# Kernel tuning notes

Hardware: AMD Instinct MI355X
Metric: run time of the kernel (lower is better)

## Reference

```python
import jax, jax.numpy as jnp
import numpy as np

N_NODES = 100000
N_EDGES = 800000
N_LAYERS = 6
GATE_TYPES = 29
H = 256        # hidden dim
INTER = 256    # inter dim
EDGE_F = 3     # (src_idx, dst_idx, reversed) edge features


def setup_inputs() -> dict:
    key = jax.random.key(0)
    ks = jax.random.split(key, 16)
    gate_type = jax.random.randint(ks[0], (N_NODES,), 0, GATE_TYPES)
    src = jax.random.randint(ks[1], (N_EDGES,), 0, N_NODES)
    dst = jax.random.randint(ks[2], (N_EDGES,), 0, N_NODES)
    w = jax.random.uniform(ks[3], (N_EDGES, EDGE_F), dtype=jnp.float32)
    s = 0.05
    emb = jax.random.normal(ks[4], (GATE_TYPES, H), dtype=jnp.float32) * s
    # QConv per layer: linear1 (no bias): [INTER, H+3]; linear2: [H, H+INTER] + bias
    W1 = jax.random.normal(ks[5], (N_LAYERS, INTER, H + EDGE_F), dtype=jnp.float32) * s
    W2 = jax.random.normal(ks[6], (N_LAYERS, H, H + INTER), dtype=jnp.float32) * s
    b2 = jax.random.normal(ks[7], (N_LAYERS, H), dtype=jnp.float32) * s
    # MLP head 256->256->1
    Wh1 = jax.random.normal(ks[8], (H, H), dtype=jnp.float32) * s
    bh1 = jax.random.normal(ks[9], (H,), dtype=jnp.float32) * s
    Wh2 = jax.random.normal(ks[10], (1, H), dtype=jnp.float32) * s
    bh2 = jax.random.normal(ks[11], (1,), dtype=jnp.float32) * s
    return {"gate_type": gate_type, "src": src, "dst": dst, "w": w,
            "emb": emb, "W1": W1, "W2": W2, "b2": b2,
            "Wh1": Wh1, "bh1": bh1, "Wh2": Wh2, "bh2": bh2}


def reference(gate_type, src, dst, w, emb, W1, W2, b2, Wh1, bh1, Wh2, bh2):
    n = gate_type.shape[0]
    h = emb[gate_type]                                   # [N, H]
    deg = jax.ops.segment_sum(jnp.ones((src.shape[0],), h.dtype), dst, num_segments=n)
    inv_deg = (1.0 / jnp.maximum(deg, 1.0))[:, None]      # mean over mailbox; 0-deg nodes -> h_N = 0
    for l in range(W1.shape[0]):
        m = jnp.concatenate([h[src], w], axis=1)          # [E, H+3] gather
        tmp = jax.nn.leaky_relu(m @ W1[l].T, 0.01)        # [E, INTER]
        h_N = jax.ops.segment_sum(tmp, dst, num_segments=n) * inv_deg  # scatter-mean [N, INTER]
        h = jax.nn.relu(jnp.concatenate([h, h_N], axis=1) @ W2[l].T + b2[l])
    x = jax.nn.relu(h @ Wh1.T + bh1)                      # [N, H]
    return x @ Wh2.T + bh2                                # [N, 1]
```

## Files before the change

### kernel.cpp

```cpp
#include <hip/hip_runtime.h>

#define H 256
#define NLAYERS 6
typedef unsigned int uint32;
typedef unsigned short u16;

typedef __bf16 bf16;
typedef bf16 bf16x8 __attribute__((ext_vector_type(8)));
typedef float f32x4 __attribute__((ext_vector_type(4)));
typedef u16 u16x8 __attribute__((ext_vector_type(8)));

__device__ __forceinline__ float bf2f(u16 h) {
    return __uint_as_float(((uint32)h) << 16);
}
__device__ __forceinline__ u16 f2bf(float f) {
    uint32 u = __float_as_uint(f);
    u = u + 0x7FFFu + ((u >> 16) & 1u);
    return (u16)(u >> 16);
}

__device__ __forceinline__ void glds16(const void* src, const char* ldsdst) {
    __builtin_amdgcn_global_load_lds(
        (const __attribute__((address_space(1))) void*)src,
        (__attribute__((address_space(3))) void*)ldsdst, 16, 0, 0);
}


__global__ __launch_bounds__(256)
void count_kernel(const int* __restrict__ dst, int* __restrict__ deg, int E) {
    int e = blockIdx.x * 256 + threadIdx.x;
    if (e < E) atomicAdd(&deg[dst[e]], 1);
}

__global__ __launch_bounds__(256)
void invd_kernel(const int* __restrict__ deg, float* __restrict__ invd, int N) {
    int n = blockIdx.x * 256 + threadIdx.x;
    if (n < N) invd[n] = 1.f / fmaxf((float)deg[n], 1.f);
}

__global__ __launch_bounds__(256)
void scan1_kernel(const int* __restrict__ deg, int* __restrict__ bsum, int N) {
    __shared__ int s[256];
    int t = threadIdx.x;
    int i = blockIdx.x * 256 + t;
    s[t] = (i < N) ? deg[i] : 0;
    __syncthreads();
    for (int off = 128; off; off >>= 1) {
        if (t < off) s[t] += s[t + off];
        __syncthreads();
    }
    if (t == 0) bsum[blockIdx.x] = s[0];
}

__global__ __launch_bounds__(512)
void scan2_kernel(int* __restrict__ bsum, int nb) {
    __shared__ int s[512];
    int t = threadIdx.x;
    int v = (t < nb) ? bsum[t] : 0;
    s[t] = v;
    __syncthreads();
    for (int off = 1; off < 512; off <<= 1) {
        int x = (t >= off) ? s[t - off] : 0;
        __syncthreads();
        s[t] += x;
        __syncthreads();
    }
    if (t < nb) bsum[t] = s[t] - v;
}

__global__ __launch_bounds__(256)
void scan3_kernel(const int* __restrict__ deg, const int* __restrict__ bsum,
                  int* __restrict__ rowptr, int N, int E) {
    __shared__ int s[256];
    int t = threadIdx.x;
    int i = blockIdx.x * 256 + t;
    int v = (i < N) ? deg[i] : 0;
    s[t] = v;
    __syncthreads();
    for (int off = 1; off < 256; off <<= 1) {
        int x = (t >= off) ? s[t - off] : 0;
        __syncthreads();
        s[t] += x;
        __syncthreads();
    }
    if (i < N) rowptr[i] = s[t] - v + bsum[blockIdx.x];
    if (i == 0) rowptr[N] = E;
}

__global__ __launch_bounds__(256)
void scatter_kernel(const int* __restrict__ src, const int* __restrict__ dst,
                    const float* __restrict__ w, const int* __restrict__ rowptr,
                    int* __restrict__ cursor, int* __restrict__ srcS,
                    float* __restrict__ wS, int E) {
    int e = blockIdx.x * 256 + threadIdx.x;
    if (e >= E) return;
    int d = dst[e];
    int p = rowptr[d] + atomicAdd(&cursor[d], 1);
    srcS[p] = src[e];
    float4 wq;
    wq.x = w[(size_t)e * 3 + 0];
    wq.y = w[(size_t)e * 3 + 1];
    wq.z = w[(size_t)e * 3 + 2];
    wq.w = 0.f;
    *(float4*)&wS[(size_t)p * 4] = wq;
}


__global__ __launch_bounds__(256)
void wsplit_kernel(const float* __restrict__ W1, const float* __restrict__ W2,
                   const float* __restrict__ Wh1,
                   u16* __restrict__ W1hi, u16* __restrict__ W1lo,
                   u16* __restrict__ W2hi, u16* __restrict__ W2lo,
                   u16* __restrict__ Wh1hi, u16* __restrict__ Wh1lo)
{
    int i = blockIdx.x * 256 + threadIdx.x;
    float v; u16* ph; u16* pl; int o;
    if (i < 393216) {
        int l = i >> 16, rem = i & 65535, r = rem >> 8, k = rem & 255;
        v = W1[(size_t)l * 66304 + (size_t)r * 259 + k];
        ph = W1hi; pl = W1lo; o = i;
    } else if (i < 1179648) {
        int j = i - 393216;
        v = W2[j];
        ph = W2hi; pl = W2lo; o = j;
    } else if (i < 1245184) {
        int j = i - 1179648;
        v = Wh1[j];
        ph = Wh1hi; pl = Wh1lo; o = j;
    } else return;
    u16 hi = f2bf(v);
    ph[o] = hi;
    pl[o] = f2bf(v - bf2f(hi));
}

__global__ void extract_kernel(const float* __restrict__ W1, float* __restrict__ ccAll)
{
    int l = blockIdx.x;
    int i = threadIdx.x;
    const float* W1l = W1 + (size_t)l * 66304;
    float* cc = ccAll + (size_t)l * 768;
    #pragma unroll
    for (int j = 0; j < 3; ++j)
        cc[j * 256 + i] = W1l[(size_t)i * 259 + 256 + j];
}


__global__ __launch_bounds__(256)
void emb_split_kernel(const int* __restrict__ gt, const float* __restrict__ emb,
                      u16* __restrict__ hHi, u16* __restrict__ hLo, int N) {
    size_t idx = (size_t)blockIdx.x * 256 + threadIdx.x;
    if (idx >= (size_t)N * 256) return;
    int n = (int)(idx >> 8), c = (int)(idx & 255);
    float v = emb[(size_t)gt[n] * 256 + c];
    u16 hi = f2bf(v);
    hHi[idx] = hi;
    hLo[idx] = f2bf(v - bf2f(hi));
}


#define LDS_AHI 0
#define LDS_ALO 8192
#define LDS_WHI 16384
#define LDS_WLO 32768
#define BUFSZ   49152

template<bool MAIN>
__device__ __forceinline__ void do_compute(const char* B, const int* aoff,
                                           const int* woff, f32x4 (&acc)[4][4]) {
    bf16x8 ah[4], al[4];
    #pragma unroll
    for (int mi = 0; mi < 4; ++mi) {
        ah[mi] = *(const bf16x8*)(B + LDS_AHI + aoff[mi]);
        if (MAIN) al[mi] = *(const bf16x8*)(B + LDS_ALO + aoff[mi]);
    }
    #pragma unroll
    for (int nj = 0; nj < 4; ++nj) {
        bf16x8 wh = *(const bf16x8*)(B + LDS_WHI + woff[nj]);
        bf16x8 wl = *(const bf16x8*)(B + LDS_WLO + woff[nj]);
        #pragma unroll
        for (int mi = 0; mi < 4; ++mi) {
            acc[mi][nj] = __builtin_amdgcn_mfma_f32_16x16x32_bf16(wh, ah[mi], acc[mi][nj], 0, 0, 0);
            acc[mi][nj] = __builtin_amdgcn_mfma_f32_16x16x32_bf16(wl, ah[mi], acc[mi][nj], 0, 0, 0);
            if (MAIN)
                acc[mi][nj] = __builtin_amdgcn_mfma_f32_16x16x32_bf16(wh, al[mi], acc[mi][nj], 0, 0, 0);
        }
    }
}

template<int KTOT, bool BIASRELU, bool WLO>
__global__ __launch_bounds__(512)
void mfma_gemm_kernel(const u16* __restrict__ Ahi_, const u16* __restrict__ Alo_,
                      const u16* __restrict__ A2_,
                      const u16* __restrict__ Whi_, const u16* __restrict__ Wlo_,
                      const float* __restrict__ bias,
                      u16* __restrict__ Chi, u16* __restrict__ Clo, int M)
{
    __shared__ __align__(128) char lds[2 * BUFSZ];
    const int tid = threadIdx.x;
    const int wv = tid >> 6;
    const int lane = tid & 63;
    const int m0 = blockIdx.x * 128;
    const int lrow = lane & 15, koct = lane >> 4;
    const int rh = wv & 1, cg = wv >> 1;

    int aoff[4], woff[4];
    #pragma unroll
    for (int mi = 0; mi < 4; ++mi) {
        int r = rh * 64 + mi * 16 + lrow;
        aoff[mi] = r * 64 + ((koct ^ ((r >> 1) & 3)) << 4);
    }
    #pragma unroll
    for (int nj = 0; nj < 4; ++nj) {
        int r = cg * 64 + nj * 16 + lrow;
        woff[nj] = r * 64 + ((koct ^ ((r >> 1) & 3)) << 4);
    }

    const int arow = tid >> 2;
    const int achk = (tid & 3) ^ ((arow >> 1) & 3);
    const long agrow = (long)((m0 + arow < M) ? (m0 + arow) : (M - 1));
    const char* Asrc_hi = (const char*)Ahi_ + agrow * 512 + achk * 16;
    const char* Asrc_lo = (const char*)Alo_ + agrow * 512 + achk * 16;
    const char* Asrc_2  = (const char*)A2_  + agrow * 512 + achk * 16;

    int wrow0 = tid >> 2,          wchk0 = (tid & 3) ^ ((wrow0 >> 1) & 3);
    int wrow1 = (512 + tid) >> 2,  wchk1 = ((512 + tid) & 3) ^ ((wrow1 >> 1) & 3);
    const char* Wsrc_h0 = (const char*)Whi_ + (long)wrow0 * (KTOT * 2) + wchk0 * 16;
    const char* Wsrc_h1 = (const char*)Whi_ + (long)wrow1 * (KTOT * 2) + wchk1 * 16;
    const char* Wsrc_l0 = (const char*)Wlo_ + (long)wrow0 * (KTOT * 2) + wchk0 * 16;
    const char* Wsrc_l1 = (const char*)Wlo_ + (long)wrow1 * (KTOT * 2) + wchk1 * 16;

    auto STAGE = [&](char* B, int t) {
        const int k0 = t * 32;
        if (KTOT == 256 || k0 < 256) {
            glds16(Asrc_hi + k0 * 2, B + LDS_AHI + wv * 1024);
            glds16(Asrc_lo + k0 * 2, B + LDS_ALO + wv * 1024);
        } else {
            glds16(Asrc_2 + (k0 - 256) * 2, B + LDS_AHI + wv * 1024);
        }
        glds16(Wsrc_h0 + k0 * 2, B + LDS_WHI + wv * 1024);
        glds16(Wsrc_h1 + k0 * 2, B + LDS_WHI + 8192 + wv * 1024);
        glds16(Wsrc_l0 + k0 * 2, B + LDS_WLO + wv * 1024);
        glds16(Wsrc_l1 + k0 * 2, B + LDS_WLO + 8192 + wv * 1024);
    };

    f32x4 acc[4][4] = {};

    char* bcur = lds;
    char* bnxt = lds + BUFSZ;

    STAGE(bcur, 0);
    asm volatile("s_waitcnt vmcnt(0)" ::: "memory");
    __builtin_amdgcn_s_barrier();
    __builtin_amdgcn_sched_barrier(0);

    const int NT = KTOT / 32;
    for (int t = 0; t < NT; ++t) {
        if (t + 1 < NT) STAGE(bnxt, t + 1);
        if (KTOT == 256 || t < 8) do_compute<true>(bcur, aoff, woff, acc);
        else                      do_compute<false>(bcur, aoff, woff, acc);
        asm volatile("s_waitcnt lgkmcnt(0) vmcnt(0)" ::: "memory");
        __builtin_amdgcn_s_barrier();
        __builtin_amdgcn_sched_barrier(0);
        char* z = bcur; bcur = bnxt; bnxt = z;
    }

    float4 bv[4];
    if (BIASRELU) {
        #pragma unroll
        for (int nj = 0; nj < 4; ++nj)
            bv[nj] = *(const float4*)&bias[cg * 64 + nj * 16 + koct * 4];
    }
    #pragma unroll
    for (int mi = 0; mi < 4; ++mi) {
        int row = m0 + rh * 64 + mi * 16 + lrow;
        if (row >= M) continue;
        #pragma unroll
        for (int nj = 0; nj < 4; ++nj) {
            f32x4 v = acc[mi][nj];
            if (BIASRELU) {
                v[0] = fmaxf(v[0] + bv[nj].x, 0.f);
                v[1] = fmaxf(v[1] + bv[nj].y, 0.f);
                v[2] = fmaxf(v[2] + bv[nj].z, 0.f);
                v[3] = fmaxf(v[3] + bv[nj].w, 0.f);
            }
            size_t o = (size_t)row * 256 + cg * 64 + nj * 16 + koct * 4;
            ushort4 ohi;
            ohi.x = f2bf(v[0]); ohi.y = f2bf(v[1]);
            ohi.z = f2bf(v[2]); ohi.w = f2bf(v[3]);
            *(ushort4*)&Chi[o] = ohi;
            if (WLO) {
                ushort4 olo;
                olo.x = f2bf(v[0] - bf2f(ohi.x));
                olo.y = f2bf(v[1] - bf2f(ohi.y));
                olo.z = f2bf(v[2] - bf2f(ohi.z));
                olo.w = f2bf(v[3] - bf2f(ohi.w));
                *(ushort4*)&Clo[o] = olo;
            }
        }
    }
}


__global__ __launch_bounds__(256)
void edge_agg_kernel(const int* __restrict__ rowptr, const int* __restrict__ srcS,
                     const float* __restrict__ wS, const u16* __restrict__ T,
                     const float* __restrict__ cc, const float* __restrict__ invd,
                     u16* __restrict__ hN, int N) {
    int n = blockIdx.x * 4 + (threadIdx.x >> 6);
    int lane = threadIdx.x & 63;
    if (n >= N) return;
    const int half = lane >> 5;
    const int c32 = lane & 31;
    const int col0 = c32 * 8;

    float c0[8], c1[8], c2[8];
    #pragma unroll
    for (int j = 0; j < 3; ++j) {
        float4 lo4 = *(const float4*)&cc[j * 256 + col0];
        float4 hi4 = *(const float4*)&cc[j * 256 + col0 + 4];
        float* cj = (j == 0) ? c0 : (j == 1) ? c1 : c2;
        cj[0] = lo4.x; cj[1] = lo4.y; cj[2] = lo4.z; cj[3] = lo4.w;
        cj[4] = hi4.x; cj[5] = hi4.y; cj[6] = hi4.z; cj[7] = hi4.w;
    }

    float acc[8] = {};
    const int e0 = rowptr[n], e1 = rowptr[n + 1];
    int e = e0 + half;
    for (; e + 6 < e1; e += 8) {
        int s0 = srcS[e], s1 = srcS[e + 2], s2 = srcS[e + 4], s3 = srcS[e + 6];
        float4 wa = *(const float4*)&wS[(size_t)e * 4];
        float4 wb = *(const float4*)&wS[(size_t)(e + 2) * 4];
        float4 wc = *(const float4*)&wS[(size_t)(e + 4) * 4];
        float4 wd = *(const float4*)&wS[(size_t)(e + 6) * 4];
        u16x8 t0 = *(const u16x8*)&T[(size_t)s0 * 256 + col0];
        u16x8 t1 = *(const u16x8*)&T[(size_t)s1 * 256 + col0];
        u16x8 t2 = *(const u16x8*)&T[(size_t)s2 * 256 + col0];
        u16x8 t3 = *(const u16x8*)&T[(size_t)s3 * 256 + col0];
        #pragma unroll
        for (int q = 0; q < 8; ++q) {
            float x0 = fmaf(wa.x, c0[q], fmaf(wa.y, c1[q], fmaf(wa.z, c2[q], bf2f(t0[q]))));
            acc[q] += (x0 > 0.f) ? x0 : 0.01f * x0;
            float x1 = fmaf(wb.x, c0[q], fmaf(wb.y, c1[q], fmaf(wb.z, c2[q], bf2f(t1[q]))));
            acc[q] += (x1 > 0.f) ? x1 : 0.01f * x1;
            float x2 = fmaf(wc.x, c0[q], fmaf(wc.y, c1[q], fmaf(wc.z, c2[q], bf2f(t2[q]))));
            acc[q] += (x2 > 0.f) ? x2 : 0.01f * x2;
            float x3 = fmaf(wd.x, c0[q], fmaf(wd.y, c1[q], fmaf(wd.z, c2[q], bf2f(t3[q]))));
            acc[q] += (x3 > 0.f) ? x3 : 0.01f * x3;
        }
    }
    for (; e < e1; e += 2) {
        int s0 = srcS[e];
        float4 wa = *(const float4*)&wS[(size_t)e * 4];
        u16x8 t0 = *(const u16x8*)&T[(size_t)s0 * 256 + col0];
        #pragma unroll
        for (int q = 0; q < 8; ++q) {
            float x = fmaf(wa.x, c0[q], fmaf(wa.y, c1[q], fmaf(wa.z, c2[q], bf2f(t0[q]))));
            acc[q] += (x > 0.f) ? x : 0.01f * x;
        }
    }
    #pragma unroll
    for (int q = 0; q < 8; ++q) acc[q] += __shfl_xor(acc[q], 32);
    if (half == 0) {
        float sc = invd[n];
        u16x8 o;
        #pragma unroll
        for (int q = 0; q < 8; ++q) o[q] = f2bf(acc[q] * sc);
        *(u16x8*)&hN[(size_t)n * 256 + col0] = o;
    }
}


__global__ __launch_bounds__(256)
void head_out_kernel(const u16* __restrict__ xhi, const u16* __restrict__ xlo,
                     const float* __restrict__ wh2,
                     const float* __restrict__ bh2, float* __restrict__ out, int N) {
    int n = blockIdx.x * 4 + (threadIdx.x >> 6);
    int lane = threadIdx.x & 63;
    if (n >= N) return;
    ushort4 hv = ((const ushort4*)(xhi + (size_t)n * H))[lane];
    ushort4 lv = ((const ushort4*)(xlo + (size_t)n * H))[lane];
    float4 wv = ((const float4*)wh2)[lane];
    float x0 = bf2f(hv.x) + bf2f(lv.x);
    float x1 = bf2f(hv.y) + bf2f(lv.y);
    float x2 = bf2f(hv.z) + bf2f(lv.z);
    float x3 = bf2f(hv.w) + bf2f(lv.w);
    float sum = x0 * wv.x + x1 * wv.y + x2 * wv.z + x3 * wv.w;
    #pragma unroll
    for (int off = 32; off; off >>= 1) sum += __shfl_xor(sum, off);
    if (lane == 0) out[n] = sum + bh2[0];
}


extern "C" void kernel_launch(void* const* d_in, const int* in_sizes, int n_in,
                              void* d_out, int out_size, void* d_ws, size_t ws_size,
                              hipStream_t stream) {
    const int*   gate_type = (const int*)d_in[0];
    const int*   src  = (const int*)d_in[1];
    const int*   dst  = (const int*)d_in[2];
    const float* w    = (const float*)d_in[3];
    const float* emb  = (const float*)d_in[4];
    const float* W1   = (const float*)d_in[5];
    const float* W2   = (const float*)d_in[6];
    const float* b2   = (const float*)d_in[7];
    const float* Wh1  = (const float*)d_in[8];
    const float* bh1  = (const float*)d_in[9];
    const float* Wh2  = (const float*)d_in[10];
    const float* bh2  = (const float*)d_in[11];
    float* out = (float*)d_out;

    const int N = in_sizes[0];
    const int E = in_sizes[1];

    char* p = (char*)d_ws;
    auto alloc = [&](size_t bytes) -> char* {
        char* r = p;
        p += (bytes + 1023) & ~(size_t)1023;
        return r;
    };
    u16*   hHi   = (u16*)  alloc((size_t)N * H * 2);
    u16*   hLo   = (u16*)  alloc((size_t)N * H * 2);
    u16*   tBuf  = (u16*)  alloc((size_t)N * H * 2);
    u16*   hNBuf = (u16*)  alloc((size_t)N * H * 2);
    int*   srcS  = (int*)  alloc((size_t)E * 4);
    float* wS    = (float*)alloc((size_t)E * 4 * 4);
    int*   rowptr= (int*)  alloc((size_t)(N + 1) * 4);
    int*   cursor= (int*)  alloc((size_t)N * 4);
    int*   bsum  = (int*)  alloc(4096);
    float* invd  = (float*)alloc((size_t)N * 4);
    float* ccAll = (float*)alloc(6u * 768 * 4);
    u16*   W1hi  = (u16*)  alloc(6u * 256 * 256 * 2);
    u16*   W1lo  = (u16*)  alloc(6u * 256 * 256 * 2);
    u16*   W2hi  = (u16*)  alloc(6u * 256 * 512 * 2);
    u16*   W2lo  = (u16*)  alloc(6u * 256 * 512 * 2);
    u16*   Wh1hi = (u16*)  alloc(256u * 256 * 2);
    u16*   Wh1lo = (u16*)  alloc(256u * 256 * 2);

    const int nb1 = (N + 255) / 256;

    hipMemsetAsync(cursor, 0, (size_t)N * 4, stream);
    count_kernel<<<(E + 255) / 256, 256, 0, stream>>>(dst, cursor, E);
    invd_kernel<<<nb1, 256, 0, stream>>>(cursor, invd, N);
    scan1_kernel<<<nb1, 256, 0, stream>>>(cursor, bsum, N);
    scan2_kernel<<<1, 512, 0, stream>>>(bsum, nb1);
    scan3_kernel<<<nb1, 256, 0, stream>>>(cursor, bsum, rowptr, N, E);
    hipMemsetAsync(cursor, 0, (size_t)N * 4, stream);
    scatter_kernel<<<(E + 255) / 256, 256, 0, stream>>>(src, dst, w, rowptr, cursor, srcS, wS, E);

    wsplit_kernel<<<4864, 256, 0, stream>>>(W1, W2, Wh1, W1hi, W1lo, W2hi, W2lo, Wh1hi, Wh1lo);
    extract_kernel<<<6, 256, 0, stream>>>(W1, ccAll);
    emb_split_kernel<<<N, 256, 0, stream>>>(gate_type, emb, hHi, hLo, N);

    const int gm = (N + 127) / 128;
    for (int l = 0; l < NLAYERS; ++l) {
        mfma_gemm_kernel<256, false, false><<<gm, 512, 0, stream>>>(
            hHi, hLo, nullptr, W1hi + (size_t)l * 65536, W1lo + (size_t)l * 65536,
            nullptr, tBuf, nullptr, N);
        edge_agg_kernel<<<(N + 3) / 4, 256, 0, stream>>>(
            rowptr, srcS, wS, tBuf, ccAll + (size_t)l * 768, invd, hNBuf, N);
        mfma_gemm_kernel<512, true, true><<<gm, 512, 0, stream>>>(
            hHi, hLo, hNBuf, W2hi + (size_t)l * 131072, W2lo + (size_t)l * 131072,
            b2 + (size_t)l * 256, hHi, hLo, N);
    }
    mfma_gemm_kernel<256, true, true><<<gm, 512, 0, stream>>>(
        hHi, hLo, nullptr, Wh1hi, Wh1lo, bh1, hHi, hLo, N);
    head_out_kernel<<<(N + 3) / 4, 256, 0, stream>>>(hHi, hLo, Wh2, bh2, out, N);
}
```

Before: 1.936 ms.

## Load GEMM A operand straight to registers and make GEMM kernel persistent

The MFMA GEMM no longer stages the activation (A) tiles through LDS. Each lane reads its bf16x8 hi/lo fragments directly from global memory, and LDS now double-buffers only the hi/lo weight tiles, which halves the LDS footprint. The kernel becomes persistent: a fixed grid of 512 blocks strides over the 128-row tiles, and launch bounds now request 4 blocks per CU. The aim is to cut LDS traffic and usage and raise occupancy. The risks are that the direct A loads are only partially coalesced and get no prefetch, so their global latency sits exposed behind the per-step vmcnt(0) wait.

```diff
diff --git a/kernel.cpp b/kernel.cpp
--- a/kernel.cpp
+++ b/kernel.cpp
@@ -158,25 +158,16 @@
 }
 
 
-#define LDS_AHI 0
-#define LDS_ALO 8192
-#define LDS_WHI 16384
-#define LDS_WLO 32768
-#define BUFSZ   49152
+#define WBUF 32768
 
 template<bool MAIN>
-__device__ __forceinline__ void do_compute(const char* B, const int* aoff,
-                                           const int* woff, f32x4 (&acc)[4][4]) {
-    bf16x8 ah[4], al[4];
-    #pragma unroll
-    for (int mi = 0; mi < 4; ++mi) {
-        ah[mi] = *(const bf16x8*)(B + LDS_AHI + aoff[mi]);
-        if (MAIN) al[mi] = *(const bf16x8*)(B + LDS_ALO + aoff[mi]);
-    }
+__device__ __forceinline__ void do_compute(const char* B, const int* woff,
+                                           const bf16x8* ah, const bf16x8* al,
+                                           f32x4 (&acc)[4][4]) {
     #pragma unroll
     for (int nj = 0; nj < 4; ++nj) {
-        bf16x8 wh = *(const bf16x8*)(B + LDS_WHI + woff[nj]);
-        bf16x8 wl = *(const bf16x8*)(B + LDS_WLO + woff[nj]);
+        bf16x8 wh = *(const bf16x8*)(B + woff[nj]);
+        bf16x8 wl = *(const bf16x8*)(B + 16384 + woff[nj]);
         #pragma unroll
         for (int mi = 0; mi < 4; ++mi) {
             acc[mi][nj] = __builtin_amdgcn_mfma_f32_16x16x32_bf16(wh, ah[mi], acc[mi][nj], 0, 0, 0);
@@ -188,113 +179,119 @@
 }
 
 template<int KTOT, bool BIASRELU, bool WLO>
-__global__ __launch_bounds__(512)
+__global__ __launch_bounds__(512, 4)
 void mfma_gemm_kernel(const u16* __restrict__ Ahi_, const u16* __restrict__ Alo_,
                       const u16* __restrict__ A2_,
                       const u16* __restrict__ Whi_, const u16* __restrict__ Wlo_,
                       const float* __restrict__ bias,
-                      u16* __restrict__ Chi, u16* __restrict__ Clo, int M)
+                      u16* __restrict__ Chi, u16* __restrict__ Clo,
+                      int M, int ntiles)
 {
-    __shared__ __align__(128) char lds[2 * BUFSZ];
+    __shared__ __align__(128) char lds[2 * WBUF];
     const int tid = threadIdx.x;
     const int wv = tid >> 6;
     const int lane = tid & 63;
-    const int m0 = blockIdx.x * 128;
     const int lrow = lane & 15, koct = lane >> 4;
     const int rh = wv & 1, cg = wv >> 1;
-
-    int aoff[4], woff[4];
-    #pragma unroll
-    for (int mi = 0; mi < 4; ++mi) {
-        int r = rh * 64 + mi * 16 + lrow;
-        aoff[mi] = r * 64 + ((koct ^ ((r >> 1) & 3)) << 4);
-    }
+    const int NT = KTOT / 32;
+
+    int woff[4];
     #pragma unroll
     for (int nj = 0; nj < 4; ++nj) {
         int r = cg * 64 + nj * 16 + lrow;
         woff[nj] = r * 64 + ((koct ^ ((r >> 1) & 3)) << 4);
     }
 
-    const int arow = tid >> 2;
-    const int achk = (tid & 3) ^ ((arow >> 1) & 3);
-    const long agrow = (long)((m0 + arow < M) ? (m0 + arow) : (M - 1));
-    const char* Asrc_hi = (const char*)Ahi_ + agrow * 512 + achk * 16;
-    const char* Asrc_lo = (const char*)Alo_ + agrow * 512 + achk * 16;
-    const char* Asrc_2  = (const char*)A2_  + agrow * 512 + achk * 16;
-
-    int wrow0 = tid >> 2,          wchk0 = (tid & 3) ^ ((wrow0 >> 1) & 3);
-    int wrow1 = (512 + tid) >> 2,  wchk1 = ((512 + tid) & 3) ^ ((wrow1 >> 1) & 3);
-    const char* Wsrc_h0 = (const char*)Whi_ + (long)wrow0 * (KTOT * 2) + wchk0 * 16;
-    const char* Wsrc_h1 = (const char*)Whi_ + (long)wrow1 * (KTOT * 2) + wchk1 * 16;
-    const char* Wsrc_l0 = (const char*)Wlo_ + (long)wrow0 * (KTOT * 2) + wchk0 * 16;
-    const char* Wsrc_l1 = (const char*)Wlo_ + (long)wrow1 * (KTOT * 2) + wchk1 * 16;
-
-    auto STAGE = [&](char* B, int t) {
-        const int k0 = t * 32;
-        if (KTOT == 256 || k0 < 256) {
-            glds16(Asrc_hi + k0 * 2, B + LDS_AHI + wv * 1024);
-            glds16(Asrc_lo + k0 * 2, B + LDS_ALO + wv * 1024);
-        } else {
-            glds16(Asrc_2 + (k0 - 256) * 2, B + LDS_AHI + wv * 1024);
-        }
-        glds16(Wsrc_h0 + k0 * 2, B + LDS_WHI + wv * 1024);
-        glds16(Wsrc_h1 + k0 * 2, B + LDS_WHI + 8192 + wv * 1024);
-        glds16(Wsrc_l0 + k0 * 2, B + LDS_WLO + wv * 1024);
-        glds16(Wsrc_l1 + k0 * 2, B + LDS_WLO + 8192 + wv * 1024);
-    };
-
-    f32x4 acc[4][4] = {};
-
-    char* bcur = lds;
-    char* bnxt = lds + BUFSZ;
-
-    STAGE(bcur, 0);
-    asm volatile("s_waitcnt vmcnt(0)" ::: "memory");
-    __builtin_amdgcn_s_barrier();
-    __builtin_amdgcn_sched_barrier(0);
-
-    const int NT = KTOT / 32;
-    for (int t = 0; t < NT; ++t) {
-        if (t + 1 < NT) STAGE(bnxt, t + 1);
-        if (KTOT == 256 || t < 8) do_compute<true>(bcur, aoff, woff, acc);
-        else                      do_compute<false>(bcur, aoff, woff, acc);
-        asm volatile("s_waitcnt lgkmcnt(0) vmcnt(0)" ::: "memory");
+    const int wrow0 = tid >> 2;
+    const int wchk0 = (tid & 3) ^ ((wrow0 >> 1) & 3);
+    const int wrow1 = 128 + (tid >> 2);
+    const int wchk1 = (tid & 3) ^ ((wrow1 >> 1) & 3);
+    const uint32 wsrc0 = (uint32)wrow0 * (KTOT * 2) + wchk0 * 16;
+    const uint32 wsrc1 = (uint32)wrow1 * (KTOT * 2) + wchk1 * 16;
+    const int ldst = wv * 1024;
+
+    for (int tile = blockIdx.x; tile < ntiles; tile += gridDim.x) {
+        const int m0 = tile * 128;
+
+        uint32 aoffB[4];
+        #pragma unroll
+        for (int mi = 0; mi < 4; ++mi) {
+            int row = m0 + rh * 64 + mi * 16 + lrow;
+            if (row > M - 1) row = M - 1;
+            aoffB[mi] = ((uint32)row * 256 + (uint32)koct * 8) * 2;
+        }
+
+        f32x4 acc[4][4] = {};
+
+        glds16((const char*)Whi_ + wsrc0, lds + ldst);
+        glds16((const char*)Whi_ + wsrc1, lds + 8192 + ldst);
+        glds16((const char*)Wlo_ + wsrc0, lds + 16384 + ldst);
+        glds16((const char*)Wlo_ + wsrc1, lds + 24576 + ldst);
+        asm volatile("s_waitcnt vmcnt(0)" ::: "memory");
         __builtin_amdgcn_s_barrier();
         __builtin_amdgcn_sched_barrier(0);
-        char* z = bcur; bcur = bnxt; bnxt = z;
-    }
-
-    float4 bv[4];
-    if (BIASRELU) {
-        #pragma unroll
-        for (int nj = 0; nj < 4; ++nj)
-            bv[nj] = *(const float4*)&bias[cg * 64 + nj * 16 + koct * 4];
-    }
-    #pragma unroll
-    for (int mi = 0; mi < 4; ++mi) {
-        int row = m0 + rh * 64 + mi * 16 + lrow;
-        if (row >= M) continue;
-        #pragma unroll
-        for (int nj = 0; nj < 4; ++nj) {
-            f32x4 v = acc[mi][nj];
-            if (BIASRELU) {
-                v[0] = fmaxf(v[0] + bv[nj].x, 0.f);
-                v[1] = fmaxf(v[1] + bv[nj].y, 0.f);
-                v[2] = fmaxf(v[2] + bv[nj].z, 0.f);
-                v[3] = fmaxf(v[3] + bv[nj].w, 0.f);
+
+        #pragma unroll
+        for (int t = 0; t < NT; ++t) {
+            const char* bcur = lds + (t & 1) * WBUF;
+            char* bnxt = lds + ((t + 1) & 1) * WBUF;
+            if (t + 1 < NT) {
+                glds16((const char*)Whi_ + wsrc0 + (t + 1) * 64, bnxt + ldst);
+                glds16((const char*)Whi_ + wsrc1 + (t + 1) * 64, bnxt + 8192 + ldst);
+                glds16((const char*)Wlo_ + wsrc0 + (t + 1) * 64, bnxt + 16384 + ldst);
+                glds16((const char*)Wlo_ + wsrc1 + (t + 1) * 64, bnxt + 24576 + ldst);
             }
-            size_t o = (size_t)row * 256 + cg * 64 + nj * 16 + koct * 4;
-            ushort4 ohi;
-            ohi.x = f2bf(v[0]); ohi.y = f2bf(v[1]);
-            ohi.z = f2bf(v[2]); ohi.w = f2bf(v[3]);
-            *(ushort4*)&Chi[o] = ohi;
-            if (WLO) {
-                ushort4 olo;
-                olo.x = f2bf(v[0] - bf2f(ohi.x));
-                olo.y = f2bf(v[1] - bf2f(ohi.y));
-                olo.z = f2bf(v[2] - bf2f(ohi.z));
-                olo.w = f2bf(v[3] - bf2f(ohi.w));
-                *(ushort4*)&Clo[o] = olo;
+            bf16x8 ah[4], al[4];
+            if (KTOT == 256 || t < 8) {
+                #pragma unroll
+                for (int mi = 0; mi < 4; ++mi) {
+                    ah[mi] = *(const bf16x8*)((const char*)Ahi_ + aoffB[mi] + t * 64);
+                    al[mi] = *(const bf16x8*)((const char*)Alo_ + aoffB[mi] + t * 64);
+                }
+                do_compute<true>(bcur, woff, ah, al, acc);
+            } else {
+                #pragma unroll
+                for (int mi = 0; mi < 4; ++mi)
+                    ah[mi] = *(const bf16x8*)((const char*)A2_ + aoffB[mi] + (t - 8) * 64);
+                do_compute<false>(bcur, woff, ah, ah, acc);
+            }
+            asm volatile("s_waitcnt lgkmcnt(0) vmcnt(0)" ::: "memory");
+            __builtin_amdgcn_s_barrier();
+            __builtin_amdgcn_sched_barrier(0);
+        }
+
+        float4 bv[4];
+        if (BIASRELU) {
+            #pragma unroll
+            for (int nj = 0; nj < 4; ++nj)
+                bv[nj] = *(const float4*)&bias[cg * 64 + nj * 16 + koct * 4];
+        }
+        #pragma unroll
+        for (int mi = 0; mi < 4; ++mi) {
+            int row = m0 + rh * 64 + mi * 16 + lrow;
+            if (row >= M) continue;
+            #pragma unroll
+            for (int nj = 0; nj < 4; ++nj) {
+                f32x4 v = acc[mi][nj];
+                if (BIASRELU) {
+                    v[0] = fmaxf(v[0] + bv[nj].x, 0.f);
+                    v[1] = fmaxf(v[1] + bv[nj].y, 0.f);
+                    v[2] = fmaxf(v[2] + bv[nj].z, 0.f);
+                    v[3] = fmaxf(v[3] + bv[nj].w, 0.f);
+                }
+                size_t o = (size_t)row * 256 + cg * 64 + nj * 16 + koct * 4;
+                ushort4 ohi;
+                ohi.x = f2bf(v[0]); ohi.y = f2bf(v[1]);
+                ohi.z = f2bf(v[2]); ohi.w = f2bf(v[3]);
+                *(ushort4*)&Chi[o] = ohi;
+                if (WLO) {
+                    ushort4 olo;
+                    olo.x = f2bf(v[0] - bf2f(ohi.x));
+                    olo.y = f2bf(v[1] - bf2f(ohi.y));
+                    olo.z = f2bf(v[2] - bf2f(ohi.z));
+                    olo.w = f2bf(v[3] - bf2f(ohi.w));
+                    *(ushort4*)&Clo[o] = olo;
+                }
             }
         }
     }
@@ -450,18 +447,19 @@
     extract_kernel<<<6, 256, 0, stream>>>(W1, ccAll);
     emb_split_kernel<<<N, 256, 0, stream>>>(gate_type, emb, hHi, hLo, N);
 
-    const int gm = (N + 127) / 128;
+    const int ntiles = (N + 127) / 128;
+    const int ggrid = 512;
     for (int l = 0; l < NLAYERS; ++l) {
-        mfma_gemm_kernel<256, false, false><<<gm, 512, 0, stream>>>(
+        mfma_gemm_kernel<256, false, false><<<ggrid, 512, 0, stream>>>(
             hHi, hLo, nullptr, W1hi + (size_t)l * 65536, W1lo + (size_t)l * 65536,
-            nullptr, tBuf, nullptr, N);
+            nullptr, tBuf, nullptr, N, ntiles);
         edge_agg_kernel<<<(N + 3) / 4, 256, 0, stream>>>(
             rowptr, srcS, wS, tBuf, ccAll + (size_t)l * 768, invd, hNBuf, N);
-        mfma_gemm_kernel<512, true, true><<<gm, 512, 0, stream>>>(
+        mfma_gemm_kernel<512, true, true><<<ggrid, 512, 0, stream>>>(
             hHi, hLo, hNBuf, W2hi + (size_t)l * 131072, W2lo + (size_t)l * 131072,
-            b2 + (size_t)l * 256, hHi, hLo, N);
-    }
-    mfma_gemm_kernel<256, true, true><<<gm, 512, 0, stream>>>(
-        hHi, hLo, nullptr, Wh1hi, Wh1lo, bh1, hHi, hLo, N);
+            b2 + (size_t)l * 256, hHi, hLo, N, ntiles);
+    }
+    mfma_gemm_kernel<256, true, true><<<ggrid, 512, 0, stream>>>(
+        hHi, hLo, nullptr, Wh1hi, Wh1lo, bh1, hHi, hLo, N, ntiles);
     head_out_kernel<<<(N + 3) / 4, 256, 0, stream>>>(hHi, hLo, Wh2, bh2, out, N);
 }
```

Result: slower. 3.543 ms (+83.1%).
